# Performance work log

Measured on AMD Instinct MI355X. Metric: run time of the kernel, lower is better.

The kernel has to match this reference:

```python
import jax, jax.numpy as jnp
import numpy as np

H_NOISE_SCALE = 0.01          # config.h_noise_scale
N_ITERS_NO_GRAD = 50          # config.nmf_inference_iters_no_grad
N_ITERS_GRAD = 10             # config.nmf_gradient_iters_with_grad


def _lipschitz(WtW, n_iters=30):
    # Largest eigenvalue of Wx^T Wx via power iteration (Lipschitz constant of the gradient).
    k = WtW.shape[0]
    v = jnp.ones((k,), WtW.dtype) / jnp.sqrt(jnp.asarray(k, WtW.dtype))

    def body(i, v):
        w = WtW @ v
        return w / (jnp.linalg.norm(w) + 1e-12)

    v = jax.lax.fori_loop(0, n_iters, body, v)
    return v @ (WtW @ v)


def _fista_right_update(x, W, h0, n_iters):
    # Solve min_{H>=0} ||x - W H||_F^2 for H^T (shape [batch, k]) with FISTA.
    WtW = W.T @ W                     # [k, k], hoisted out of the loop
    XtW = x.T @ W                     # [batch, k]
    inv_L = 1.0 / _lipschitz(WtW)

    def step(carry, _):
        h, y, t = carry
        grad = y @ WtW - XtW          # d/dH^T of 0.5||x - W H||^2
        h_new = jnp.maximum(y - grad * inv_L, 0.0)   # proximal step (nonneg projection)
        t_new = 0.5 * (1.0 + jnp.sqrt(1.0 + 4.0 * t * t))
        y_new = h_new + ((t - 1.0) / t_new) * (h_new - h)
        return (h_new, y_new, t_new), None

    t0 = jnp.asarray(1.0, x.dtype)
    (h, _, _), _ = jax.lax.scan(step, (h0, h0, t0), None, length=n_iters)
    return h


def setup_inputs() -> dict:
    key = jax.random.key(0)
    k1, k2, k3, k4 = jax.random.split(key, 4)
    x_dim, y_dim, k, batch = 784, 10, 1024, 2048
    x = jax.random.uniform(k1, (x_dim, batch), dtype=jnp.float32)
    Wx = jax.random.uniform(k2, (x_dim, k), dtype=jnp.float32) * 0.02
    Wy = jax.random.uniform(k3, (y_dim, k), dtype=jnp.float32) * 0.02
    h_init = jax.random.uniform(k4, (batch, k), dtype=jnp.float32) * H_NOISE_SCALE
    return {"x": x, "Wx": Wx, "Wy": Wy, "h_init": h_init}


def reference(x, Wx, Wy, h_init):
    # Phase 1: no-grad FISTA warm start (torch.no_grad() -> stop_gradient).
    h = jax.lax.stop_gradient(_fista_right_update(x, Wx, h_init, N_ITERS_NO_GRAD))
    # Phase 2: differentiated FISTA iterations.
    h = _fista_right_update(x, Wx, h, N_ITERS_GRAD)
    # y_pred = einsum('ij,kj->ik', Wy, h_tran): shape [y_dim, batch]
    return jnp.einsum('ij,kj->ik', Wy, h)
```

## Files before the change

### kernel.cpp

```cpp
#include <hip/hip_runtime.h>
#include <math.h>

#define KD    1024
#define BATCH 2048
#define XD    784
#define YD    10

typedef _Float16 f16;
typedef _Float16 f16x8 __attribute__((ext_vector_type(8)));
typedef _Float16 f16x4 __attribute__((ext_vector_type(4)));
typedef float    f32x4 __attribute__((ext_vector_type(4)));

__device__ __forceinline__ void gll16(const void* g, void* l)
{
    __builtin_amdgcn_global_load_lds(
        (const __attribute__((address_space(1))) void*)g,
        (__attribute__((address_space(3))) void*)l,
        16, 0, 0);
}

#define TS  64
#define KS  32
#define LDP 68

__device__ __forceinline__ void atb_body(const float* __restrict__ A,
                                         const float* __restrict__ B,
                                         float* __restrict__ C,
                                         int M, int N, int K, int bx, int by,
                                         float (*As)[LDP], float (*Bs)[LDP])
{
    const int tid = threadIdx.x;
    const int tx = tid & 15, ty = tid >> 4;
    const int i0 = by * TS, j0 = bx * TS;
    float acc[4][4] = {};

    for (int k0 = 0; k0 < K; k0 += KS) {
#pragma unroll
        for (int q = 0; q < 2; ++q) {
            const int f  = tid + q * 256;
            const int kr = f >> 4;
            const int cc = (f & 15) << 2;
            float4 av = make_float4(0.f, 0.f, 0.f, 0.f);
            float4 bv = av;
            if (k0 + kr < K) {
                av = *(const float4*)(A + (size_t)(k0 + kr) * M + i0 + cc);
                bv = *(const float4*)(B + (size_t)(k0 + kr) * N + j0 + cc);
            }
            *(float4*)&As[kr][cc] = av;
            *(float4*)&Bs[kr][cc] = bv;
        }
        __syncthreads();
#pragma unroll
        for (int kk = 0; kk < KS; ++kk) {
            const float4 a4 = *(const float4*)&As[kk][ty << 2];
            const float4 b4 = *(const float4*)&Bs[kk][tx << 2];
            const float a[4] = {a4.x, a4.y, a4.z, a4.w};
            const float b[4] = {b4.x, b4.y, b4.z, b4.w};
#pragma unroll
            for (int r = 0; r < 4; ++r)
#pragma unroll
                for (int c = 0; c < 4; ++c)
                    acc[r][c] = fmaf(a[r], b[c], acc[r][c]);
        }
        __syncthreads();
    }
#pragma unroll
    for (int r = 0; r < 4; ++r) {
        float4 o = make_float4(acc[r][0], acc[r][1], acc[r][2], acc[r][3]);
        *(float4*)(C + (size_t)(i0 + (ty << 2) + r) * N + j0 + (tx << 2)) = o;
    }
}

__global__ __launch_bounds__(256) void setup_fused(const float* __restrict__ x,
                                                   const float* __restrict__ Wx,
                                                   const float* __restrict__ h_init,
                                                   float* __restrict__ WtW,
                                                   float* __restrict__ XtW,
                                                   f16* __restrict__ h0f,
                                                   float* __restrict__ w0)
{
    __shared__ float As[KS][LDP];
    __shared__ float Bs[KS][LDP];
    const int blk = blockIdx.x;
    if (blk < 256) {
        atb_body(Wx, Wx, WtW, KD, KD, XD, blk & 15, blk >> 4, As, Bs);
    } else if (blk < 768) {
        const int l = blk - 256;
        atb_body(x, Wx, XtW, BATCH, KD, XD, l & 15, l >> 4, As, Bs);
    } else if (blk < 1792) {
        const int i = (blk - 768) * 256 + threadIdx.x;
        const f32x4 a = ((const f32x4*)h_init)[2 * i];
        const f32x4 b = ((const f32x4*)h_init)[2 * i + 1];
        f16x8 o;
#pragma unroll
        for (int j = 0; j < 4; ++j) { o[j] = (f16)a[j]; o[j + 4] = (f16)b[j]; }
        ((f16x8*)h0f)[i] = o;
    } else {
        ((float4*)w0)[threadIdx.x] = make_float4(0.03125f, 0.03125f, 0.03125f, 0.03125f);
    }
}

__global__ __launch_bounds__(256) void convert_fused(const float* __restrict__ WtW,
                                                     const float* __restrict__ XtW,
                                                     f16* __restrict__ bhi,
                                                     f16* __restrict__ xth,
                                                     f16* __restrict__ xtl)
{
    const int blk = blockIdx.x;
    if (blk < 512) {
        const int i = blk * 256 + threadIdx.x;
        const f32x4 a = ((const f32x4*)WtW)[2 * i];
        const f32x4 b = ((const f32x4*)WtW)[2 * i + 1];
        f16x8 o;
#pragma unroll
        for (int j = 0; j < 4; ++j) {
            o[j]     = (f16)(256.0f * a[j]);
            o[j + 4] = (f16)(256.0f * b[j]);
        }
        ((f16x8*)bhi)[i] = o;
    } else {
        const int i = (blk - 512) * 256 + threadIdx.x;
        const float4 v = ((const float4*)XtW)[i];
        const f16 h0 = (f16)v.x, h1 = (f16)v.y, h2 = (f16)v.z, h3 = (f16)v.w;
        f16x4 hv = {h0, h1, h2, h3};
        f16x4 lv = {(f16)(v.x - (float)h0), (f16)(v.y - (float)h1),
                    (f16)(v.z - (float)h2), (f16)(v.w - (float)h3)};
        ((f16x4*)xth)[i] = hv;
        ((f16x4*)xtl)[i] = lv;
    }
}

#define BMF 128
#define BNF 64
#define A_OFF 131072

__global__ __launch_bounds__(512, 1) void fista160(
    const f16* __restrict__ yhP,
    const f16* __restrict__ hhP,
    const f16* __restrict__ bhiP,
    const f16* __restrict__ xthP,
    const f16* __restrict__ xtlP,
    const float* __restrict__ invLp, float cm,
    f16* __restrict__ HO, f16* __restrict__ YO)
{
    __shared__ char lds[163840];

    const int t    = threadIdx.x;
    const int lane = t & 63;
    const int wid  = t >> 6;
    const int wm   = wid >> 1;
    const int wn   = wid & 1;
    const int lr   = lane & 15;
    const int lk   = (lane >> 4) * 8;

    const int bid = blockIdx.y * gridDim.x + blockIdx.x;
    const int xc  = bid & 7, j = bid >> 3;
    const int m0  = ((xc >> 1) * 4 + (j >> 3)) * BMF;
    const int n0  = ((xc & 1) * 8 + (j & 7)) * BNF;

#pragma unroll
    for (int i = 0; i < 16; ++i) {
        const int c = wid * 16 + i;
        const int kt = c >> 3, u = c & 7;
        const int g = u & 3, s = u >> 2;
        gll16(bhiP + (size_t)(n0 + 16 * g + lr) * KD + kt * 64 + s * 32 + lk,
              lds + c * 1024 + lane * 16);
    }

    auto stageA = [&](int buf, int kt) {
#pragma unroll
        for (int i = 0; i < 2; ++i) {
            const int a = wid * 2 + i;
            const int g = a & 7, s = a >> 3;
            gll16(yhP + (size_t)(m0 + 16 * g + lr) * KD + kt * 64 + 32 * s + lk,
                  lds + A_OFF + buf * 16384 + a * 1024 + lane * 16);
        }
    };

    stageA(0, 0);
    asm volatile("s_waitcnt vmcnt(0)" ::: "memory");
    __builtin_amdgcn_s_barrier();
    asm volatile("" ::: "memory");

    f32x4 acc[2][2] = {};

#pragma unroll
    for (int kt = 0; kt < 16; ++kt) {
        const int buf = kt & 1;
        if (kt < 15) stageA(buf ^ 1, kt + 1);

        f16x8 Af[2][2], Bf[2][2];
#pragma unroll
        for (int s = 0; s < 2; ++s) {
#pragma unroll
            for (int f = 0; f < 2; ++f)
                Af[s][f] = *(const f16x8*)(lds + A_OFF + buf * 16384
                                           + ((s << 3) + wm * 2 + f) * 1024 + lane * 16);
#pragma unroll
            for (int b = 0; b < 2; ++b)
                Bf[s][b] = *(const f16x8*)(lds + (kt * 8 + (s << 2) + wn * 2 + b) * 1024
                                           + lane * 16);
        }
#pragma unroll
        for (int s = 0; s < 2; ++s)
#pragma unroll
            for (int f = 0; f < 2; ++f)
#pragma unroll
                for (int b = 0; b < 2; ++b)
                    acc[f][b] = __builtin_amdgcn_mfma_f32_16x16x32_f16(Af[s][f], Bf[s][b], acc[f][b], 0, 0, 0);

        if (kt < 15) { asm volatile("s_waitcnt vmcnt(0)" ::: "memory"); }
        __builtin_amdgcn_s_barrier();
        asm volatile("" ::: "memory");
    }

    float* eb = (float*)lds;
#pragma unroll
    for (int f = 0; f < 2; ++f)
#pragma unroll
        for (int b = 0; b < 2; ++b) {
            const int r0 = wm * 32 + 16 * f + 4 * (lane >> 4);
            const int cl = wn * 32 + 16 * b + lr;
#pragma unroll
            for (int r = 0; r < 4; ++r)
                eb[(r0 + r) * 68 + cl] = acc[f][b][r];
        }
    __syncthreads();

    const int row = t >> 2;
    const int cb  = (t & 3) * 16;
    const float invL  = invLp[0];
    const float invLs = invL * 0.00390625f;
    const size_t gb = (size_t)(m0 + row) * KD + n0 + cb;
    {
        const f32x4 a0 = *(const f32x4*)(eb + row * 68 + cb);
        const f32x4 a1 = *(const f32x4*)(eb + row * 68 + cb + 4);
        const f32x4 a2 = *(const f32x4*)(eb + row * 68 + cb + 8);
        const f32x4 a3 = *(const f32x4*)(eb + row * 68 + cb + 12);
        const f16x8 yh8a = *(const f16x8*)(yhP + gb);
        const f16x8 yh8b = *(const f16x8*)(yhP + gb + 8);
        const f16x8 hh8a = *(const f16x8*)(hhP + gb);
        const f16x8 hh8b = *(const f16x8*)(hhP + gb + 8);
        const f16x8 xh8a = *(const f16x8*)(xthP + gb);
        const f16x8 xh8b = *(const f16x8*)(xthP + gb + 8);
        const f16x8 xl8a = *(const f16x8*)(xtlP + gb);
        const f16x8 xl8b = *(const f16x8*)(xtlP + gb + 8);
        f16x8 oha, ohb, oya, oyb;
#pragma unroll
        for (int jj = 0; jj < 8; ++jj) {
            const float av = (jj < 4) ? a0[jj] : a1[jj - 4];
            const float xv = (float)xh8a[jj] + (float)xl8a[jj];
            const float yv = (float)yh8a[jj];
            const float hv = (float)hh8a[jj];
            const float t1 = fmaf(invL, xv, yv);
            const float hn = fmaxf(fmaf(-invLs, av, t1), 0.f);
            const float yn = fmaf(cm, hn - hv, hn);
            oha[jj] = (f16)hn;
            oya[jj] = (f16)yn;
        }
#pragma unroll
        for (int jj = 0; jj < 8; ++jj) {
            const float av = (jj < 4) ? a2[jj] : a3[jj - 4];
            const float xv = (float)xh8b[jj] + (float)xl8b[jj];
            const float yv = (float)yh8b[jj];
            const float hv = (float)hh8b[jj];
            const float t1 = fmaf(invL, xv, yv);
            const float hn = fmaxf(fmaf(-invLs, av, t1), 0.f);
            const float yn = fmaf(cm, hn - hv, hn);
            ohb[jj] = (f16)hn;
            oyb[jj] = (f16)yn;
        }
        *(f16x8*)(HO + gb)     = oha;
        *(f16x8*)(HO + gb + 8) = ohb;
        *(f16x8*)(YO + gb)     = oya;
        *(f16x8*)(YO + gb + 8) = oyb;
    }
}

__global__ __launch_bounds__(256) void matvec_n_kernel(const float* __restrict__ WtW,
                                                       const float* __restrict__ win,
                                                       float* __restrict__ wout)
{
    __shared__ float red[4];
    __shared__ float invnS;
    const int t = threadIdx.x;
    const int wave = t >> 6, lane = t & 63;

    const float4 wv = *(const float4*)(win + t * 4);
    float ss = wv.x * wv.x + wv.y * wv.y + wv.z * wv.z + wv.w * wv.w;
#pragma unroll
    for (int off = 32; off > 0; off >>= 1) ss += __shfl_down(ss, off);
    if (lane == 0) red[wave] = ss;
    __syncthreads();
    if (t == 0) invnS = 1.0f / (sqrtf(red[0] + red[1] + red[2] + red[3]) + 1e-12f);
    __syncthreads();
    const float invn = invnS;

    const int row = blockIdx.x * 4 + wave;
    const float* rp = WtW + (size_t)row * KD;
    float s = 0.f;
#pragma unroll
    for (int q = 0; q < KD / 64; ++q)
        s = fmaf(rp[lane + 64 * q], win[lane + 64 * q] * invn, s);
#pragma unroll
    for (int off = 32; off > 0; off >>= 1) s += __shfl_down(s, off);
    if (lane == 0) wout[row] = s;
}

__global__ __launch_bounds__(1024) void rayleigh_n_kernel(const float* __restrict__ wprev,
                                                          const float* __restrict__ wlast,
                                                          float* __restrict__ invL)
{
    __shared__ float red[16];
    __shared__ float invnS;
    const int t = threadIdx.x;
    const float a = wprev[t];
    float ss = a * a;
#pragma unroll
    for (int off = 32; off > 0; off >>= 1) ss += __shfl_down(ss, off);
    if ((t & 63) == 0) red[t >> 6] = ss;
    __syncthreads();
    if (t < 64) {
        float v = (t < 16) ? red[t] : 0.f;
#pragma unroll
        for (int off = 8; off > 0; off >>= 1) v += __shfl_down(v, off);
        if (t == 0) invnS = 1.0f / (sqrtf(v) + 1e-12f);
    }
    __syncthreads();
    float s = (a * invnS) * wlast[t];
#pragma unroll
    for (int off = 32; off > 0; off >>= 1) s += __shfl_down(s, off);
    __syncthreads();
    if ((t & 63) == 0) red[t >> 6] = s;
    __syncthreads();
    if (t == 0) {
        float tot = 0.f;
#pragma unroll
        for (int i = 0; i < 16; ++i) tot += red[i];
        invL[0] = 1.0f / tot;
    }
}

__global__ __launch_bounds__(256) void ypred_kernel(const float* __restrict__ Wy,
                                                    const f16* __restrict__ hh,
                                                    float* __restrict__ out)
{
    const int wave = threadIdx.x >> 6;
    const int lane = threadIdx.x & 63;
    const int b    = blockIdx.x * 4 + wave;
    float p[YD] = {};
    const f16* hp = hh + (size_t)b * KD;
#pragma unroll 4
    for (int q = 0; q < KD / 64; ++q) {
        const int j = lane + 64 * q;
        const float hv = (float)hp[j];
#pragma unroll
        for (int i = 0; i < YD; ++i)
            p[i] = fmaf(Wy[i * KD + j], hv, p[i]);
    }
#pragma unroll
    for (int i = 0; i < YD; ++i) {
        float s = p[i];
#pragma unroll
        for (int off = 32; off > 0; off >>= 1)
            s += __shfl_down(s, off);
        if (lane == 0) out[(size_t)i * BATCH + b] = s;
    }
}

extern "C" void kernel_launch(void* const* d_in, const int* in_sizes, int n_in,
                              void* d_out, int out_size, void* d_ws, size_t ws_size,
                              hipStream_t stream)
{
    const float* x      = (const float*)d_in[0];
    const float* Wx     = (const float*)d_in[1];
    const float* Wy     = (const float*)d_in[2];
    const float* h_init = (const float*)d_in[3];
    float* out = (float*)d_out;

    char* base = (char*)d_ws;
    const size_t MB = 1 << 20;
    float* WtW  = (float*)(base + 0 * MB);
    float* XtW  = (float*)(base + 4 * MB);
    f16* bhiP   = (f16*)(base + 12 * MB);
    f16* xthP   = (f16*)(base + 14 * MB);
    f16* xtlP   = (f16*)(base + 18 * MB);
    f16* h0f    = (f16*)(base + 22 * MB);
    f16* hA     = (f16*)(base + 26 * MB);
    f16* yA     = (f16*)(base + 30 * MB);
    f16* hB     = (f16*)(base + 34 * MB);
    f16* yB     = (f16*)(base + 38 * MB);
    float* wA   = (float*)(base + 42 * MB);
    float* wB   = (float*)(base + 42 * MB + 8192);
    float* invL = (float*)(base + 42 * MB + 16384);

    setup_fused<<<1793, 256, 0, stream>>>(x, Wx, h_init, WtW, XtW, h0f, wA);

    convert_fused<<<2560, 256, 0, stream>>>(WtW, XtW, bhiP, xthP, xtlP);

    float* wcur = wA; float* wnxt = wB;
    for (int it = 0; it < 5; ++it) {
        matvec_n_kernel<<<KD / 4, 256, 0, stream>>>(WtW, wcur, wnxt);
        float* tmp = wcur; wcur = wnxt; wnxt = tmp;
    }
    rayleigh_n_kernel<<<1, 1024, 0, stream>>>(wA, wB, invL);

    float t = 1.0f;
    const f16 *yin = h0f, *hin = h0f;
    int outSel = 1;
    for (int n = 0; n < 60; ++n) {
        if (n == 50) { t = 1.0f; yin = hin; }
        const float tn = 0.5f * (1.0f + sqrtf(1.0f + 4.0f * t * t));
        const float cm = (t - 1.0f) / tn;
        f16* ho = outSel ? hA : hB;
        f16* yo = outSel ? yA : yB;
        fista160<<<dim3(KD / BNF, BATCH / BMF), 512, 0, stream>>>(
            yin, hin, bhiP, xthP, xtlP, invL, cm, ho, yo);
        t = tn;
        hin = ho; yin = yo;
        outSel ^= 1;
    }

    ypred_kernel<<<BATCH / 4, 256, 0, stream>>>(Wy, hin, out);
}
```

Measured before the change: 1.316 ms.

## Compute setup Gram products with split-f16 MFMA and fuse conversion into epilogue

Replaces the scalar fp32 FMA tiles that compute Wx^T Wx and x^T Wx with MFMA f16 matrix instructions. Inputs are scaled and split into hi/lo halves, and three MFMA products are summed to approximate fp32 accuracy. The f16 conversion of WtW and XtW is fused into the GEMM epilogue, which removes the separate convert kernel and the fp32 XtW buffer round trip. The risk is small accuracy loss from the split-f16 emulation and uncoalesced scalar f16 epilogue stores.

New measurement: 1.294 ms. No clear change (-1.6%).

```diff
diff --git a/kernel.cpp b/kernel.cpp
--- a/kernel.cpp
+++ b/kernel.cpp
@@ -19,115 +19,140 @@
         16, 0, 0);
 }
 
-#define TS  64
-#define KS  32
-#define LDP 68
-
-__device__ __forceinline__ void atb_body(const float* __restrict__ A,
-                                         const float* __restrict__ B,
-                                         float* __restrict__ C,
-                                         int M, int N, int K, int bx, int by,
-                                         float (*As)[LDP], float (*Bs)[LDP])
-{
-    const int tid = threadIdx.x;
-    const int tx = tid & 15, ty = tid >> 4;
-    const int i0 = by * TS, j0 = bx * TS;
-    float acc[4][4] = {};
-
-    for (int k0 = 0; k0 < K; k0 += KS) {
-#pragma unroll
-        for (int q = 0; q < 2; ++q) {
-            const int f  = tid + q * 256;
-            const int kr = f >> 4;
-            const int cc = (f & 15) << 2;
-            float4 av = make_float4(0.f, 0.f, 0.f, 0.f);
-            float4 bv = av;
-            if (k0 + kr < K) {
-                av = *(const float4*)(A + (size_t)(k0 + kr) * M + i0 + cc);
-                bv = *(const float4*)(B + (size_t)(k0 + kr) * N + j0 + cc);
-            }
-            *(float4*)&As[kr][cc] = av;
-            *(float4*)&Bs[kr][cc] = bv;
-        }
-        __syncthreads();
-#pragma unroll
-        for (int kk = 0; kk < KS; ++kk) {
-            const float4 a4 = *(const float4*)&As[kk][ty << 2];
-            const float4 b4 = *(const float4*)&Bs[kk][tx << 2];
-            const float a[4] = {a4.x, a4.y, a4.z, a4.w};
-            const float b[4] = {b4.x, b4.y, b4.z, b4.w};
-#pragma unroll
-            for (int r = 0; r < 4; ++r)
-#pragma unroll
-                for (int c = 0; c < 4; ++c)
-                    acc[r][c] = fmaf(a[r], b[c], acc[r][c]);
-        }
-        __syncthreads();
-    }
-#pragma unroll
-    for (int r = 0; r < 4; ++r) {
-        float4 o = make_float4(acc[r][0], acc[r][1], acc[r][2], acc[r][3]);
-        *(float4*)(C + (size_t)(i0 + (ty << 2) + r) * N + j0 + (tx << 2)) = o;
-    }
-}
-
-__global__ __launch_bounds__(256) void setup_fused(const float* __restrict__ x,
-                                                   const float* __restrict__ Wx,
-                                                   const float* __restrict__ h_init,
-                                                   float* __restrict__ WtW,
-                                                   float* __restrict__ XtW,
-                                                   f16* __restrict__ h0f,
-                                                   float* __restrict__ w0)
-{
-    __shared__ float As[KS][LDP];
-    __shared__ float Bs[KS][LDP];
+#define SST 80
+
+__global__ __launch_bounds__(256) void setup16(const float* __restrict__ x,
+                                               const float* __restrict__ Wx,
+                                               const float* __restrict__ h_init,
+                                               float* __restrict__ WtW,
+                                               f16* __restrict__ bhi,
+                                               f16* __restrict__ xth,
+                                               f16* __restrict__ xtl,
+                                               f16* __restrict__ h0f,
+                                               float* __restrict__ w0)
+{
     const int blk = blockIdx.x;
-    if (blk < 256) {
-        atb_body(Wx, Wx, WtW, KD, KD, XD, blk & 15, blk >> 4, As, Bs);
-    } else if (blk < 768) {
-        const int l = blk - 256;
-        atb_body(x, Wx, XtW, BATCH, KD, XD, l & 15, l >> 4, As, Bs);
-    } else if (blk < 1792) {
-        const int i = (blk - 768) * 256 + threadIdx.x;
+    const int t   = threadIdx.x;
+
+    if (blk >= 1792) {
+        ((float4*)w0)[t] = make_float4(0.03125f, 0.03125f, 0.03125f, 0.03125f);
+        return;
+    }
+    if (blk >= 768) {
+        const int i = (blk - 768) * 256 + t;
         const f32x4 a = ((const f32x4*)h_init)[2 * i];
         const f32x4 b = ((const f32x4*)h_init)[2 * i + 1];
         f16x8 o;
 #pragma unroll
         for (int j = 0; j < 4; ++j) { o[j] = (f16)a[j]; o[j + 4] = (f16)b[j]; }
         ((f16x8*)h0f)[i] = o;
-    } else {
-        ((float4*)w0)[threadIdx.x] = make_float4(0.03125f, 0.03125f, 0.03125f, 0.03125f);
-    }
-}
-
-__global__ __launch_bounds__(256) void convert_fused(const float* __restrict__ WtW,
-                                                     const float* __restrict__ XtW,
-                                                     f16* __restrict__ bhi,
-                                                     f16* __restrict__ xth,
-                                                     f16* __restrict__ xtl)
-{
-    const int blk = blockIdx.x;
-    if (blk < 512) {
-        const int i = blk * 256 + threadIdx.x;
-        const f32x4 a = ((const f32x4*)WtW)[2 * i];
-        const f32x4 b = ((const f32x4*)WtW)[2 * i + 1];
-        f16x8 o;
-#pragma unroll
-        for (int j = 0; j < 4; ++j) {
-            o[j]     = (f16)(256.0f * a[j]);
-            o[j + 4] = (f16)(256.0f * b[j]);
-        }
-        ((f16x8*)bhi)[i] = o;
-    } else {
-        const int i = (blk - 512) * 256 + threadIdx.x;
-        const float4 v = ((const float4*)XtW)[i];
-        const f16 h0 = (f16)v.x, h1 = (f16)v.y, h2 = (f16)v.z, h3 = (f16)v.w;
-        f16x4 hv = {h0, h1, h2, h3};
-        f16x4 lv = {(f16)(v.x - (float)h0), (f16)(v.y - (float)h1),
-                    (f16)(v.z - (float)h2), (f16)(v.w - (float)h3)};
-        ((f16x4*)xth)[i] = hv;
-        ((f16x4*)xtl)[i] = lv;
-    }
+        return;
+    }
+
+    const bool isW = (blk < 256);
+    const float* A; const float* B; int M, N, i0, j0;
+    if (isW) { A = Wx; B = Wx; M = KD;    N = KD; i0 = (blk >> 4) * 64;         j0 = (blk & 15) * 64; }
+    else     { A = x;  B = Wx; M = BATCH; N = KD; i0 = ((blk - 256) >> 4) * 64; j0 = ((blk - 256) & 15) * 64; }
+
+    __shared__ char sm[4 * 64 * SST];
+    char* Ah = sm;
+    char* Al = sm + 64 * SST;
+    char* Bh = sm + 2 * 64 * SST;
+    char* Bl = sm + 3 * 64 * SST;
+
+    const int lane = t & 63, wid = t >> 6;
+    const int wm = wid >> 1, wn = wid & 1;
+    const int lg = lane >> 4, lr = lane & 15;
+
+    const bool doB = (t >= 128);
+    const int tt  = t & 127;
+    const int su  = tt >> 4;
+    const int sc4 = (tt & 15) * 4;
+    const float* src = doB ? B : A;
+    const int sw     = doB ? N : M;
+    const int sbase  = doB ? j0 : i0;
+    char* dsth = doB ? Bh : Ah;
+    char* dstl = doB ? Bl : Al;
+
+    f32x4 acc[2][2] = {};
+
+#pragma unroll 1
+    for (int k0 = 0; k0 < 800; k0 += 32) {
+        float4 r[4];
+#pragma unroll
+        for (int dk = 0; dk < 4; ++dk) {
+            const int k = k0 + 4 * su + dk;
+            r[dk] = (k < XD) ? *(const float4*)(src + (size_t)k * sw + sbase + sc4)
+                             : make_float4(0.f, 0.f, 0.f, 0.f);
+        }
+        __syncthreads();
+#pragma unroll
+        for (int j2 = 0; j2 < 4; ++j2) {
+            const int c = sc4 + j2;
+            f16x4 h4, l4;
+#pragma unroll
+            for (int dk = 0; dk < 4; ++dk) {
+                const float v = ((const float*)&r[dk])[j2] * 256.0f;
+                const f16 hi = (f16)v;
+                const f16 lo = (f16)(v - (float)hi);
+                h4[dk] = hi;
+                l4[dk] = lo;
+            }
+            *(f16x4*)(dsth + c * SST + su * 8) = h4;
+            *(f16x4*)(dstl + c * SST + su * 8) = l4;
+        }
+        __syncthreads();
+
+        f16x8 Afh[2], Afl[2], Bfh[2], Bfl[2];
+#pragma unroll
+        for (int f = 0; f < 2; ++f) {
+            const int m = wm * 32 + f * 16 + lr;
+            Afh[f] = *(const f16x8*)(Ah + m * SST + 16 * lg);
+            Afl[f] = *(const f16x8*)(Al + m * SST + 16 * lg);
+        }
+#pragma unroll
+        for (int b = 0; b < 2; ++b) {
+            const int c = wn * 32 + b * 16 + lr;
+            Bfh[b] = *(const f16x8*)(Bh + c * SST + 16 * lg);
+            Bfl[b] = *(const f16x8*)(Bl + c * SST + 16 * lg);
+        }
+#pragma unroll
+        for (int f = 0; f < 2; ++f)
+#pragma unroll
+            for (int b = 0; b < 2; ++b)
+                acc[f][b] = __builtin_amdgcn_mfma_f32_16x16x32_f16(Afl[f], Bfh[b], acc[f][b], 0, 0, 0);
+#pragma unroll
+        for (int f = 0; f < 2; ++f)
+#pragma unroll
+            for (int b = 0; b < 2; ++b)
+                acc[f][b] = __builtin_amdgcn_mfma_f32_16x16x32_f16(Afh[f], Bfl[b], acc[f][b], 0, 0, 0);
+#pragma unroll
+        for (int f = 0; f < 2; ++f)
+#pragma unroll
+            for (int b = 0; b < 2; ++b)
+                acc[f][b] = __builtin_amdgcn_mfma_f32_16x16x32_f16(Afh[f], Bfh[b], acc[f][b], 0, 0, 0);
+    }
+
+#pragma unroll
+    for (int f = 0; f < 2; ++f)
+#pragma unroll
+        for (int b = 0; b < 2; ++b)
+#pragma unroll
+            for (int r2 = 0; r2 < 4; ++r2) {
+                const int row = i0 + wm * 32 + 16 * f + 4 * lg + r2;
+                const int col = j0 + wn * 32 + 16 * b + lr;
+                const float av = acc[f][b][r2];
+                if (isW) {
+                    bhi[(size_t)row * KD + col] = (f16)(av * 0.00390625f);
+                    WtW[(size_t)row * KD + col] = av * 1.52587890625e-05f;
+                } else {
+                    const float sv = av * 1.52587890625e-05f;
+                    const f16 hi = (f16)sv;
+                    const f16 lo = (f16)(sv - (float)hi);
+                    xth[(size_t)row * KD + col] = hi;
+                    xtl[(size_t)row * KD + col] = lo;
+                }
+            }
 }
 
 #define BMF 128
@@ -381,22 +406,19 @@
     char* base = (char*)d_ws;
     const size_t MB = 1 << 20;
     float* WtW  = (float*)(base + 0 * MB);
-    float* XtW  = (float*)(base + 4 * MB);
-    f16* bhiP   = (f16*)(base + 12 * MB);
-    f16* xthP   = (f16*)(base + 14 * MB);
-    f16* xtlP   = (f16*)(base + 18 * MB);
-    f16* h0f    = (f16*)(base + 22 * MB);
-    f16* hA     = (f16*)(base + 26 * MB);
-    f16* yA     = (f16*)(base + 30 * MB);
-    f16* hB     = (f16*)(base + 34 * MB);
-    f16* yB     = (f16*)(base + 38 * MB);
-    float* wA   = (float*)(base + 42 * MB);
-    float* wB   = (float*)(base + 42 * MB + 8192);
-    float* invL = (float*)(base + 42 * MB + 16384);
-
-    setup_fused<<<1793, 256, 0, stream>>>(x, Wx, h_init, WtW, XtW, h0f, wA);
-
-    convert_fused<<<2560, 256, 0, stream>>>(WtW, XtW, bhiP, xthP, xtlP);
+    f16* bhiP   = (f16*)(base + 4 * MB);
+    f16* xthP   = (f16*)(base + 6 * MB);
+    f16* xtlP   = (f16*)(base + 10 * MB);
+    f16* h0f    = (f16*)(base + 14 * MB);
+    f16* hA     = (f16*)(base + 18 * MB);
+    f16* yA     = (f16*)(base + 22 * MB);
+    f16* hB     = (f16*)(base + 26 * MB);
+    f16* yB     = (f16*)(base + 30 * MB);
+    float* wA   = (float*)(base + 34 * MB);
+    float* wB   = (float*)(base + 34 * MB + 8192);
+    float* invL = (float*)(base + 34 * MB + 16384);
+
+    setup16<<<1793, 256, 0, stream>>>(x, Wx, h_init, WtW, bhiP, xthP, xtlP, h0f, wA);
 
     float* wcur = wA; float* wnxt = wB;
     for (int it = 0; it < 5; ++it) {
```
